# Kernel optimization log

Measured on AMD Instinct MI355X. Metric: run time of the kernel, lower is better.

The kernel has to match this reference:

```python
import jax, jax.numpy as jnp
import numpy as np

H = 16        # num query heads
HKV = 1       # num key/value heads (MQA; source matmul broadcasts only for 1 or H)
D = 128       # head_dim
SCALE = 1.0 / np.sqrt(D)


def setup_inputs() -> dict:
    key = jax.random.key(0)
    k1, k2, k3 = jax.random.split(key, 3)
    B, S, HID = 2, 2048, 2048
    hidden_states = jax.random.normal(k1, (B, S, HID), dtype=jnp.float32)
    # real RoPE tables: cos/sin of shape [S, D]
    inv_freq = 1.0 / (10000.0 ** (np.arange(0, D, 2, dtype=np.float32) / D))
    t = np.arange(S, dtype=np.float32)
    freqs = np.outer(t, inv_freq)                      # [S, D/2]
    emb = np.concatenate([freqs, freqs], axis=-1)      # [S, D]
    cos = jnp.asarray(np.cos(emb), dtype=jnp.float32)
    sin = jnp.asarray(np.sin(emb), dtype=jnp.float32)
    w_qkv = jax.random.normal(k2, (HID, (H + 2 * HKV) * D), dtype=jnp.float32) * (HID ** -0.5)
    w_o = jax.random.normal(k3, (H * D, HID), dtype=jnp.float32) * ((H * D) ** -0.5)
    return {"hidden_states": hidden_states, "cos": cos, "sin": sin,
            "w_qkv": w_qkv, "w_o": w_o}


def _rotate_half(x):
    x1, x2 = jnp.split(x, 2, axis=-1)
    return jnp.concatenate([-x2, x1], axis=-1)


def reference(hidden_states, cos, sin, w_qkv, w_o):
    B, S, _ = hidden_states.shape
    qkv = hidden_states @ w_qkv                        # [B,S,(H+2*HKV)*D]
    qkv = qkv.reshape(B, S, H + 2 * HKV, D)
    q = qkv[:, :, :H]                                  # [B,S,H,D]
    k = qkv[:, :, H:H + HKV]                           # [B,S,HKV,D]
    v = qkv[:, :, H + HKV:]                            # [B,S,HKV,D]
    c = cos[None, :, None, :]                          # [1,S,1,D]
    s = sin[None, :, None, :]
    q = q * c + _rotate_half(q) * s
    k = k * c + _rotate_half(k) * s
    # MQA: squeeze the single kv head
    k0 = k[:, :, 0]                                    # [B,S,D]
    v0 = v[:, :, 0]                                    # [B,S,D]
    qh = jnp.transpose(q, (0, 2, 1, 3))                # [B,H,S,D]
    scores = jnp.einsum('bhsd,btd->bhst', qh, k0) * SCALE
    attn = jax.nn.softmax(scores.astype(jnp.float32), axis=-1).astype(qh.dtype)
    out = jnp.einsum('bhst,btd->bhsd', attn, v0)       # [B,H,S,D]
    out = jnp.transpose(out, (0, 2, 1, 3)).reshape(B, S, H * D)
    return out @ w_o
```

## Files before the change

### kernel.cpp

```cpp
#include <hip/hip_runtime.h>

typedef __attribute__((ext_vector_type(8))) short bf16x8;
typedef __attribute__((ext_vector_type(4))) float f32x4;
typedef __attribute__((ext_vector_type(8))) unsigned short u16x8;
typedef __attribute__((ext_vector_type(2))) unsigned int u32x2;

#define H_Q   16
#define NH    18
#define SEQ   2048
#define BATCH 2
#define HID   2048
#define NQKV  2304
#define QK_SCALE2 0.1275174313f

__device__ __forceinline__ float bf2f(unsigned short u){
  union { unsigned int u; float f; } x; x.u = ((unsigned int)u) << 16; return x.f;
}
__device__ __forceinline__ unsigned short f2bf(float f){
  union { float f; unsigned int u; } x; x.f = f;
  unsigned int r = x.u + 0x7fffu + ((x.u >> 16) & 1u);
  return (unsigned short)(r >> 16);
}
__device__ __forceinline__ unsigned int cvtpk(float lo, float hi){
  unsigned int r;
  asm("v_cvt_pk_bf16_f32 %0, %1, %2" : "=v"(r) : "v"(lo), "v"(hi));
  return r;
}

__global__ __launch_bounds__(256) void convert_bf16(const float* __restrict__ src,
                                                    unsigned short* __restrict__ dst){
  const size_t i0 = ((size_t)blockIdx.x * 256 + threadIdx.x) * 16;
  f32x4 a = *(const f32x4*)(src + i0);
  f32x4 b = *(const f32x4*)(src + i0 + 4);
  f32x4 c = *(const f32x4*)(src + i0 + 8);
  f32x4 d = *(const f32x4*)(src + i0 + 12);
  u16x8 lo, hi;
#pragma unroll
  for (int j = 0; j < 4; ++j){
    lo[j] = f2bf(a[j]); lo[4+j] = f2bf(b[j]);
    hi[j] = f2bf(c[j]); hi[4+j] = f2bf(d[j]);
  }
  *(u16x8*)(dst + i0)     = lo;
  *(u16x8*)(dst + i0 + 8) = hi;
}

__global__ __launch_bounds__(256) void transpose_f2b(const float* __restrict__ W,
                                                     unsigned short* __restrict__ WT,
                                                     int K, int N){
  __shared__ float tile[64][72];
  const int t = threadIdx.x;
  const int nt = blockIdx.x * 64, kt = blockIdx.y * 64;
#pragma unroll
  for (int p = 0; p < 2; ++p){
    int slot = p*256 + t, r = slot >> 3, c = (slot & 7) * 8;
    *(f32x4*)&tile[r][c]     = *(const f32x4*)(W + (size_t)(kt + r)*N + nt + c);
    *(f32x4*)&tile[r][c + 4] = *(const f32x4*)(W + (size_t)(kt + r)*N + nt + c + 4);
  }
  __syncthreads();
#pragma unroll
  for (int p = 0; p < 2; ++p){
    int slot = p*256 + t, r = slot >> 3, c = (slot & 7) * 8;
    u16x8 v;
#pragma unroll
    for (int j = 0; j < 8; ++j) v[j] = f2bf(tile[c + j][r]);
    *(u16x8*)(WT + (size_t)(nt + r)*K + kt + c) = v;
  }
}

template<bool F32OUT>
__global__ __launch_bounds__(256, 2) void gemm_bt(const unsigned short* __restrict__ A,
                                                  const unsigned short* __restrict__ Bt,
                                                  void* __restrict__ Cv,
                                                  int M, int N, int K){
  __shared__ unsigned short lds[2][2][128*32];
  const int tid  = threadIdx.x;
  const int wave = tid >> 6, lane = tid & 63;
  const int row0 = blockIdx.x * 128, col0 = blockIdx.y * 128;
  const int wr = (wave >> 1) * 64, wc = (wave & 1) * 64;
  const int lm = lane & 15, lk = (lane >> 4) * 8;
  f32x4 acc[4][4] = {};

  auto stage = [&](int buf, int kt){
#pragma unroll
    for (int i = 0; i < 2; ++i){
      int slot = i*256 + tid;
      int r = slot >> 2, kc = (slot & 3) * 8;
      const unsigned short* ga = A  + (size_t)(row0 + r)*K + kt*32 + kc;
      const unsigned short* gb = Bt + (size_t)(col0 + r)*K + kt*32 + kc;
      unsigned short* la = &lds[buf][0][(i*256 + (wave << 6)) * 8];
      unsigned short* lb = &lds[buf][1][(i*256 + (wave << 6)) * 8];
      __builtin_amdgcn_global_load_lds((const __attribute__((address_space(1))) void*)ga,
                                       (__attribute__((address_space(3))) void*)la, 16, 0, 0);
      __builtin_amdgcn_global_load_lds((const __attribute__((address_space(1))) void*)gb,
                                       (__attribute__((address_space(3))) void*)lb, 16, 0, 0);
    }
  };

  stage(0, 0);
  const int KT = K >> 5;
  int buf = 0;
  for (int kt = 0; kt < KT; ++kt){
    __syncthreads();
    if (kt + 1 < KT) stage(buf ^ 1, kt + 1);
    const unsigned short* la = lds[buf][0];
    const unsigned short* lb = lds[buf][1];
    bf16x8 af[4], bfr[4];
#pragma unroll
    for (int i = 0; i < 4; ++i) af[i]  = *(const bf16x8*)&la[(wr + i*16 + lm)*32 + lk];
#pragma unroll
    for (int j = 0; j < 4; ++j) bfr[j] = *(const bf16x8*)&lb[(wc + j*16 + lm)*32 + lk];
#pragma unroll
    for (int i = 0; i < 4; ++i)
#pragma unroll
      for (int j = 0; j < 4; ++j)
        acc[i][j] = __builtin_amdgcn_mfma_f32_16x16x32_bf16(af[i], bfr[j], acc[i][j], 0, 0, 0);
    buf ^= 1;
  }

#pragma unroll
  for (int i = 0; i < 4; ++i){
    int row = row0 + wr + i*16 + (lane >> 4) * 4;
#pragma unroll
    for (int j = 0; j < 4; ++j){
      int col = col0 + wc + j*16 + lm;
#pragma unroll
      for (int r = 0; r < 4; ++r){
        if (F32OUT) ((float*)Cv)[(size_t)(row + r)*N + col] = acc[i][j][r];
        else ((unsigned short*)Cv)[(size_t)(row + r)*N + col] = f2bf(acc[i][j][r]);
      }
    }
  }
}

__global__ __launch_bounds__(256) void rope_pack(unsigned short* __restrict__ qkv,
                                                 const float* __restrict__ cosb,
                                                 const float* __restrict__ sinb,
                                                 unsigned short* __restrict__ Kb,
                                                 unsigned short* __restrict__ Vt){
  const int bs = blockIdx.x;
  const int s = bs & (SEQ-1), b = bs >> 11;
  const int t = threadIdx.x;
  unsigned short* row = qkv + (size_t)bs * NQKV;
  const float* cr = cosb + (size_t)s * 128;
  const float* sr = sinb + (size_t)s * 128;
  const int h = t >> 4, d0 = (t & 15) * 4;
  unsigned short* q = row + h * 128;
#pragma unroll
  for (int i = 0; i < 4; ++i){
    int d = d0 + i;
    float c  = cr[d], sn = sr[d];
    float x1 = bf2f(q[d]),  x2 = bf2f(q[d + 64]);
    q[d]      = f2bf((x1*c - x2*sn) * QK_SCALE2);
    q[d + 64] = f2bf((x2*c + x1*sn) * QK_SCALE2);
  }
  if (t < 64){
    const unsigned short* kk = row + H_Q*128;
    int d = t;
    float c  = cr[d], sn = sr[d];
    float x1 = bf2f(kk[d]), x2 = bf2f(kk[d + 64]);
    unsigned short* ko = Kb + ((size_t)b*SEQ + s)*128;
    ko[d]      = f2bf(x1*c - x2*sn);
    ko[d + 64] = f2bf(x2*c + x1*sn);
  }
  if (t < 128){
    Vt[((size_t)b*128 + t)*SEQ + s] = row[(H_Q + 1)*128 + t];
  }
}

__global__ __launch_bounds__(256, 2) void attn_fwd(const unsigned short* __restrict__ qkv,
                                                   const unsigned short* __restrict__ Kb,
                                                   const unsigned short* __restrict__ Vt,
                                                   unsigned short* __restrict__ Ob){
  __shared__ unsigned short kls[2][32*128];
  __shared__ unsigned short vls[2][128*32];
  const int tid = threadIdx.x, lane = tid & 63;
  const int g = lane >> 4, m = lane & 15;
  const int wg = blockIdx.x;
  const int bh = wg >> 4, qb = wg & 15;
  const int b = bh >> 4, h = bh & 15;
  const int q0 = qb * 128 + (tid >> 6) * 32;

  const unsigned short* qrowA = qkv + ((size_t)((b << 11) + q0 + m)*NH + h)*128;
  const unsigned short* qrowB = qrowA + (size_t)16*NH*128;
  bf16x8 qfA[4], qfB[4];
#pragma unroll
  for (int dc = 0; dc < 4; ++dc){
    qfA[dc] = *(const bf16x8*)(qrowA + dc*32 + g*8);
    qfB[dc] = *(const bf16x8*)(qrowB + dc*32 + g*8);
  }

  const unsigned short* Kbase = Kb + (size_t)b*SEQ*128;
  const unsigned short* Vbase = Vt + (size_t)b*128*SEQ;

  const int krow = tid >> 4;
  const int kchunk = (tid & 15) ^ (krow & 7);
  const int vrow = tid >> 2;
  const int vchunk = (tid & 3) ^ ((tid >> 3) & 3);

  auto stage = [&](int buf, int n0){
#pragma unroll
    for (int ck = 0; ck < 2; ++ck){
      const unsigned short* gp = Kbase + (size_t)(n0 + ck*16 + krow)*128 + kchunk*8;
      unsigned short* lp = &kls[buf][(ck*256 + tid) * 8];
      __builtin_amdgcn_global_load_lds((const __attribute__((address_space(1))) void*)gp,
                                       (__attribute__((address_space(3))) void*)lp, 16, 0, 0);
    }
#pragma unroll
    for (int cv = 0; cv < 2; ++cv){
      const unsigned short* gp = Vbase + (size_t)(cv*64 + vrow)*SEQ + n0 + vchunk*8;
      unsigned short* lp = &vls[buf][(cv*256 + tid) * 8];
      __builtin_amdgcn_global_load_lds((const __attribute__((address_space(1))) void*)gp,
                                       (__attribute__((address_space(3))) void*)lp, 16, 0, 0);
    }
  };

  f32x4 oA[8] = {}, oB[8] = {};
  float sA = 0.f, sB = 0.f;
  const int ksw = (m & 7);
  const int vsw = (m >> 1) & 3;

  stage(0, 0);
  const int NT = SEQ / 32;
  for (int t = 0; t < NT; ++t){
    const int cur = t & 1;
    __syncthreads();
    if (t + 1 < NT) stage(cur ^ 1, (t + 1) * 32);

    const unsigned short* kb = kls[cur];
    const unsigned short* vb = vls[cur];

    bf16x8 kf[8];
#pragma unroll
    for (int dc = 0; dc < 4; ++dc){
      kf[dc]     = *(const bf16x8*)&kb[(size_t)m*128 + ((dc*4 + g) ^ ksw)*8];
      kf[4 + dc] = *(const bf16x8*)&kb[(size_t)(16 + m)*128 + ((dc*4 + g) ^ ksw)*8];
    }

    f32x4 a0 = {0,0,0,0}, a1 = {0,0,0,0}, c0 = {0,0,0,0}, c1 = {0,0,0,0};
    __builtin_amdgcn_s_setprio(1);
#pragma unroll
    for (int dc = 0; dc < 4; ++dc){
      a0 = __builtin_amdgcn_mfma_f32_16x16x32_bf16(kf[dc], qfA[dc], a0, 0, 0, 0);
      c0 = __builtin_amdgcn_mfma_f32_16x16x32_bf16(kf[dc], qfB[dc], c0, 0, 0, 0);
    }
#pragma unroll
    for (int dc = 0; dc < 4; ++dc){
      a1 = __builtin_amdgcn_mfma_f32_16x16x32_bf16(kf[4 + dc], qfA[dc], a1, 0, 0, 0);
      c1 = __builtin_amdgcn_mfma_f32_16x16x32_bf16(kf[4 + dc], qfB[dc], c1, 0, 0, 0);
    }
    __builtin_amdgcn_s_setprio(0);

    bf16x8 vf[8];
#pragma unroll
    for (int dt = 0; dt < 8; ++dt)
      vf[dt] = *(const bf16x8*)&vb[(size_t)(dt*16 + m)*32 + ((g ^ vsw))*8];

    float pA0[4], pA1[4], pB0[4], pB1[4];
#pragma unroll
    for (int r = 0; r < 4; ++r){
      pA0[r] = exp2f(fminf(a0[r], 100.f)); sA += pA0[r];
      pA1[r] = exp2f(fminf(a1[r], 100.f)); sA += pA1[r];
      pB0[r] = exp2f(fminf(c0[r], 100.f)); sB += pB0[r];
      pB1[r] = exp2f(fminf(c1[r], 100.f)); sB += pB1[r];
    }

    unsigned int A01 = cvtpk(pA0[0], pA0[1]), A23 = cvtpk(pA0[2], pA0[3]);
    unsigned int A45 = cvtpk(pA1[0], pA1[1]), A67 = cvtpk(pA1[2], pA1[3]);
    u32x2 tA0 = __builtin_amdgcn_permlane32_swap(A01, A45, false, false);
    u32x2 wA02 = __builtin_amdgcn_permlane16_swap(tA0[0], tA0[1], false, false);
    u32x2 tA1 = __builtin_amdgcn_permlane32_swap(A23, A67, false, false);
    u32x2 wA13 = __builtin_amdgcn_permlane16_swap(tA1[0], tA1[1], false, false);
    union { unsigned int w[4]; bf16x8 v; } UA;
    UA.w[0] = wA02[0]; UA.w[1] = wA13[0]; UA.w[2] = wA02[1]; UA.w[3] = wA13[1];
    bf16x8 pfA = UA.v;

    unsigned int B01 = cvtpk(pB0[0], pB0[1]), B23 = cvtpk(pB0[2], pB0[3]);
    unsigned int B45 = cvtpk(pB1[0], pB1[1]), B67 = cvtpk(pB1[2], pB1[3]);
    u32x2 tB0 = __builtin_amdgcn_permlane32_swap(B01, B45, false, false);
    u32x2 wB02 = __builtin_amdgcn_permlane16_swap(tB0[0], tB0[1], false, false);
    u32x2 tB1 = __builtin_amdgcn_permlane32_swap(B23, B67, false, false);
    u32x2 wB13 = __builtin_amdgcn_permlane16_swap(tB1[0], tB1[1], false, false);
    union { unsigned int w[4]; bf16x8 v; } UB;
    UB.w[0] = wB02[0]; UB.w[1] = wB13[0]; UB.w[2] = wB02[1]; UB.w[3] = wB13[1];
    bf16x8 pfB = UB.v;

    __builtin_amdgcn_s_setprio(1);
#pragma unroll
    for (int dt = 0; dt < 8; ++dt){
      oA[dt] = __builtin_amdgcn_mfma_f32_16x16x32_bf16(pfA, vf[dt], oA[dt], 0, 0, 0);
      oB[dt] = __builtin_amdgcn_mfma_f32_16x16x32_bf16(pfB, vf[dt], oB[dt], 0, 0, 0);
    }
    __builtin_amdgcn_s_setprio(0);
  }

  sA += __shfl_xor(sA, 16); sA += __shfl_xor(sA, 32);
  sB += __shfl_xor(sB, 16); sB += __shfl_xor(sB, 32);
  float invA = 1.f / sA, invB = 1.f / sB;
  float ivA[4], ivB[4];
#pragma unroll
  for (int r = 0; r < 4; ++r){
    ivA[r] = __shfl(invA, g*4 + r);
    ivB[r] = __shfl(invB, g*4 + r);
  }
  unsigned short* orowA = Ob + (size_t)((b << 11) + q0)*HID + h*128;
  unsigned short* orowB = orowA + (size_t)16*HID;
#pragma unroll
  for (int dt = 0; dt < 8; ++dt)
#pragma unroll
    for (int r = 0; r < 4; ++r){
      orowA[(size_t)(g*4 + r)*HID + dt*16 + m] = f2bf(oA[dt][r] * ivA[r]);
      orowB[(size_t)(g*4 + r)*HID + dt*16 + m] = f2bf(oB[dt][r] * ivB[r]);
    }
}

extern "C" void kernel_launch(void* const* d_in, const int* in_sizes, int n_in,
                              void* d_out, int out_size, void* d_ws, size_t ws_size,
                              hipStream_t stream){
  const float* hidden = (const float*)d_in[0];
  const float* cosb   = (const float*)d_in[1];
  const float* sinb   = (const float*)d_in[2];
  const float* wqkv   = (const float*)d_in[3];
  const float* wo     = (const float*)d_in[4];
  float* out = (float*)d_out;

  char* ws = (char*)d_ws;
  unsigned short* qkvb  = (unsigned short*)ws; ws += (size_t)BATCH*SEQ*NQKV*2;
  unsigned short* hidb  = (unsigned short*)ws; ws += (size_t)BATCH*SEQ*HID*2;
  unsigned short* attnb = hidb;
  unsigned short* Kbf   = (unsigned short*)ws; ws += (size_t)BATCH*SEQ*128*2;
  unsigned short* Vt    = (unsigned short*)ws; ws += (size_t)BATCH*SEQ*128*2;
  unsigned short* wqkvT = (unsigned short*)ws; ws += (size_t)NQKV*HID*2;
  unsigned short* woT   = wqkvT;

  convert_bf16<<<dim3(BATCH*SEQ*HID/4096), 256, 0, stream>>>(hidden, hidb);
  transpose_f2b<<<dim3(NQKV/64, HID/64), 256, 0, stream>>>(wqkv, wqkvT, HID, NQKV);
  gemm_bt<false><<<dim3(BATCH*SEQ/128, NQKV/128), 256, 0, stream>>>(hidb, wqkvT, qkvb,
                                                                    BATCH*SEQ, NQKV, HID);
  rope_pack<<<dim3(BATCH*SEQ), 256, 0, stream>>>(qkvb, cosb, sinb, Kbf, Vt);
  transpose_f2b<<<dim3(HID/64, HID/64), 256, 0, stream>>>(wo, woT, HID, HID);
  attn_fwd<<<dim3(SEQ/128 * BATCH*H_Q), 256, 0, stream>>>(qkvb, Kbf, Vt, attnb);
  gemm_bt<true><<<dim3(BATCH*SEQ/128, HID/128), 256, 0, stream>>>(attnb, woT, out,
                                                                  BATCH*SEQ, HID, HID);
}
```

Before: 212.7 us.

## Split attention over the key sequence and merge partial outputs in a separate kernel

The attention kernel now splits the 2048-key range into two halves, launching twice as many workgroups. Each one writes a normalized bf16 partial output plus its softmax denominator, and a new merge kernel combines the two halves weighted by their sums. The launch bound asks for 4 workgroups per SIMD instead of 2, to raise occupancy and hide latency. In exchange it adds partial-output traffic to global memory, an extra kernel launch, an extra bf16 rounding step, and a risk of register spilling under the tighter launch bound.

Result: slower. 656.0 us (+208.5%).

```diff
diff --git a/kernel.cpp b/kernel.cpp
--- a/kernel.cpp
+++ b/kernel.cpp
@@ -11,6 +11,7 @@
 #define BATCH 2
 #define HID   2048
 #define NQKV  2304
+#define SPLIT 2
 #define QK_SCALE2 0.1275174313f
 
 __device__ __forceinline__ float bf2f(unsigned short u){
@@ -167,18 +168,21 @@
   }
 }
 
-__global__ __launch_bounds__(256, 2) void attn_fwd(const unsigned short* __restrict__ qkv,
-                                                   const unsigned short* __restrict__ Kb,
-                                                   const unsigned short* __restrict__ Vt,
-                                                   unsigned short* __restrict__ Ob){
+__global__ __launch_bounds__(256, 4) void attn_fwd_split(const unsigned short* __restrict__ qkv,
+                                                         const unsigned short* __restrict__ Kb,
+                                                         const unsigned short* __restrict__ Vt,
+                                                         unsigned short* __restrict__ Opart,
+                                                         float* __restrict__ Sarr){
   __shared__ unsigned short kls[2][32*128];
   __shared__ unsigned short vls[2][128*32];
   const int tid = threadIdx.x, lane = tid & 63;
   const int g = lane >> 4, m = lane & 15;
-  const int wg = blockIdx.x;
+  const int si = blockIdx.x >> 9;
+  const int wg = blockIdx.x & 511;
   const int bh = wg >> 4, qb = wg & 15;
   const int b = bh >> 4, h = bh & 15;
   const int q0 = qb * 128 + (tid >> 6) * 32;
+  const int n_base = si << 10;
 
   const unsigned short* qrowA = qkv + ((size_t)((b << 11) + q0 + m)*NH + h)*128;
   const unsigned short* qrowB = qrowA + (size_t)16*NH*128;
@@ -219,12 +223,12 @@
   const int ksw = (m & 7);
   const int vsw = (m >> 1) & 3;
 
-  stage(0, 0);
-  const int NT = SEQ / 32;
+  stage(0, n_base);
+  const int NT = (SEQ / SPLIT) / 32;
   for (int t = 0; t < NT; ++t){
     const int cur = t & 1;
     __syncthreads();
-    if (t + 1 < NT) stage(cur ^ 1, (t + 1) * 32);
+    if (t + 1 < NT) stage(cur ^ 1, n_base + (t + 1) * 32);
 
     const unsigned short* kb = kls[cur];
     const unsigned short* vb = vls[cur];
@@ -302,7 +306,10 @@
     ivA[r] = __shfl(invA, g*4 + r);
     ivB[r] = __shfl(invB, g*4 + r);
   }
-  unsigned short* orowA = Ob + (size_t)((b << 11) + q0)*HID + h*128;
+  float* srow = Sarr + ((size_t)si*BATCH*H_Q + bh)*SEQ + q0;
+  if (g == 0){ srow[m] = sA; srow[16 + m] = sB; }
+  unsigned short* orowA = Opart + (size_t)si*BATCH*SEQ*HID
+                        + (size_t)((b << 11) + q0)*HID + h*128;
   unsigned short* orowB = orowA + (size_t)16*HID;
 #pragma unroll
   for (int dt = 0; dt < 8; ++dt)
@@ -311,6 +318,28 @@
       orowA[(size_t)(g*4 + r)*HID + dt*16 + m] = f2bf(oA[dt][r] * ivA[r]);
       orowB[(size_t)(g*4 + r)*HID + dt*16 + m] = f2bf(oB[dt][r] * ivB[r]);
     }
+}
+
+__global__ __launch_bounds__(256) void merge_split(const unsigned short* __restrict__ Opart,
+                                                   const float* __restrict__ Sarr,
+                                                   unsigned short* __restrict__ attnb){
+  const size_t e = (size_t)blockIdx.x * 256 + threadIdx.x;
+  const size_t o = e * 8;
+  const int col = (int)(o & (HID-1));
+  const size_t row = o >> 11;
+  const int q = (int)(row & (SEQ-1)), b = (int)(row >> 11);
+  const int h = col >> 7;
+  const int bh = b*H_Q + h;
+  float s0 = Sarr[((size_t)bh)*SEQ + q];
+  float s1 = Sarr[((size_t)BATCH*H_Q + bh)*SEQ + q];
+  float inv = 1.f / (s0 + s1);
+  float w0 = s0 * inv, w1 = s1 * inv;
+  u16x8 x0 = *(const u16x8*)(Opart + o);
+  u16x8 x1 = *(const u16x8*)(Opart + (size_t)BATCH*SEQ*HID + o);
+  u16x8 y;
+#pragma unroll
+  for (int j = 0; j < 8; ++j) y[j] = f2bf(bf2f(x0[j])*w0 + bf2f(x1[j])*w1);
+  *(u16x8*)(attnb + o) = y;
 }
 
 extern "C" void kernel_launch(void* const* d_in, const int* in_sizes, int n_in,
@@ -331,6 +360,8 @@
   unsigned short* Vt    = (unsigned short*)ws; ws += (size_t)BATCH*SEQ*128*2;
   unsigned short* wqkvT = (unsigned short*)ws; ws += (size_t)NQKV*HID*2;
   unsigned short* woT   = wqkvT;
+  unsigned short* Opart = (unsigned short*)ws; ws += (size_t)SPLIT*BATCH*SEQ*HID*2;
+  float* Sarr = (float*)ws; ws += (size_t)SPLIT*BATCH*H_Q*SEQ*4;
 
   convert_bf16<<<dim3(BATCH*SEQ*HID/4096), 256, 0, stream>>>(hidden, hidb);
   transpose_f2b<<<dim3(NQKV/64, HID/64), 256, 0, stream>>>(wqkv, wqkvT, HID, NQKV);
@@ -338,7 +369,9 @@
                                                                     BATCH*SEQ, NQKV, HID);
   rope_pack<<<dim3(BATCH*SEQ), 256, 0, stream>>>(qkvb, cosb, sinb, Kbf, Vt);
   transpose_f2b<<<dim3(HID/64, HID/64), 256, 0, stream>>>(wo, woT, HID, HID);
-  attn_fwd<<<dim3(SEQ/128 * BATCH*H_Q), 256, 0, stream>>>(qkvb, Kbf, Vt, attnb);
+  attn_fwd_split<<<dim3(SPLIT * SEQ/128 * BATCH*H_Q), 256, 0, stream>>>(qkvb, Kbf, Vt,
+                                                                        Opart, Sarr);
+  merge_split<<<dim3(BATCH*SEQ*HID/2048), 256, 0, stream>>>(Opart, Sarr, attnb);
   gemm_bt<true><<<dim3(BATCH*SEQ/128, HID/128), 256, 0, stream>>>(attnb, woT, out,
                                                                   BATCH*SEQ, HID, HID);
 }
```
